# Kernel optimization log

Measured on AMD Instinct MI355X. Metric: run time of the kernel, lower is better.

The kernel has to match this reference:

```python
import jax, jax.numpy as jnp
import numpy as np

NHEADS = 4


def mha(q, k, v, w_in, b_in, w_out, b_out):
    # torch.nn.MultiheadAttention (batch_first): packed in_proj then out_proj
    B, Nq, E = q.shape
    d = E // NHEADS
    wq, wk, wv = jnp.split(w_in, 3, axis=0)
    bq, bk, bv = jnp.split(b_in, 3)
    qh = (q @ wq.T + bq).reshape(B, Nq, NHEADS, d)
    kh = (k @ wk.T + bk).reshape(B, k.shape[1], NHEADS, d)
    vh = (v @ wv.T + bv).reshape(B, v.shape[1], NHEADS, d)
    scores = jnp.einsum('bqhd,bkhd->bhqk', qh, kh) * (1.0 / np.float32(np.sqrt(d)))
    attn = jax.nn.softmax(scores, axis=-1)
    out = jnp.einsum('bhqk,bkhd->bqhd', attn, vh).reshape(B, Nq, E)
    return out @ w_out.T + b_out


def kabsch(A, B):
    # n_dim_rigid_transform_Kabsch_3D_torch; note: reflect() in the source sets
    # SS = identity on BOTH branches, so it is a no-op and R = U @ Vt exactly.
    cA = A.mean(1, keepdims=True)   # [B,1,3]
    cB = B.mean(1, keepdims=True)
    Am = A - cA
    Bm = B - cB
    H = jnp.einsum('bni,bnj->bij', Bm, Am)  # Bm^T @ Am, [B,3,3]
    U, S, Vt = jnp.linalg.svd(H, full_matrices=False)
    R = U @ Vt
    t = cA - cB @ R
    return R, t


def setup_inputs() -> dict:
    key = jax.random.key(0)
    ks = jax.random.split(key, 32)
    B, N, F, E = 64, 512, 16, 12

    def p(k, shape, s=0.1):
        return jax.random.normal(k, shape, jnp.float32) * s

    inp = {}
    inp['x_orig'] = jax.random.normal(ks[0], (B, N, F), jnp.float32)
    inp['y_orig'] = jax.random.normal(ks[1], (B, N, F), jnp.float32)
    inp['lin_in_w'] = p(ks[2], (E, F - 3))
    inp['lin_in_b'] = p(ks[3], (E,))
    inp['lin_coords_w'] = p(ks[4], (E, 3))
    inp['lin_coords_b'] = p(ks[5], (E,))
    for i, name in enumerate(['attn', 'attn_feat', 'cross_cf', 'cross']):
        b = 6 + 4 * i
        inp[name + '_w_in'] = p(ks[b], (3 * E, E))
        inp[name + '_b_in'] = p(ks[b + 1], (3 * E,))
        inp[name + '_w_out'] = p(ks[b + 2], (E, E))
        inp[name + '_b_out'] = p(ks[b + 3], (E,))
    inp['lin_out_w'] = p(ks[22], (3, E))
    inp['lin_out_b'] = p(ks[23], (3,))
    return inp


def reference(x_orig, y_orig,
              lin_in_w, lin_in_b, lin_coords_w, lin_coords_b,
              attn_w_in, attn_b_in, attn_w_out, attn_b_out,
              attn_feat_w_in, attn_feat_b_in, attn_feat_w_out, attn_feat_b_out,
              cross_cf_w_in, cross_cf_b_in, cross_cf_w_out, cross_cf_b_out,
              cross_w_in, cross_b_in, cross_w_out, cross_b_out,
              lin_out_w, lin_out_b):
    x_coords = x_orig[:, :, :3]
    x_feat = x_orig[:, :, 3:]
    y_coords = y_orig[:, :, :3]
    y_feat = y_orig[:, :, 3:]

    x_coords = x_coords - x_coords.mean(1, keepdims=True)
    y_translate = y_coords.mean(1, keepdims=True)
    y_coords = y_coords - y_translate

    xi = x_coords @ lin_coords_w.T + lin_coords_b
    yi = y_coords @ lin_coords_w.T + lin_coords_b
    xi_feat = x_feat @ lin_in_w.T + lin_in_b
    yi_feat = y_feat @ lin_in_w.T + lin_in_b

    xi_feat = mha(xi_feat, xi_feat, xi_feat, attn_feat_w_in, attn_feat_b_in, attn_feat_w_out, attn_feat_b_out)
    yi_feat = mha(yi_feat, yi_feat, yi_feat, attn_feat_w_in, attn_feat_b_in, attn_feat_w_out, attn_feat_b_out)
    xi = mha(xi, xi, xi, attn_w_in, attn_b_in, attn_w_out, attn_b_out)
    yi = mha(yi, yi, yi, attn_w_in, attn_b_in, attn_w_out, attn_b_out)

    cross_x = mha(xi, xi_feat, xi_feat, cross_cf_w_in, cross_cf_b_in, cross_cf_w_out, cross_cf_b_out)
    cross_y = mha(yi, yi_feat, yi_feat, cross_cf_w_in, cross_cf_b_in, cross_cf_w_out, cross_cf_b_out)
    cross = mha(cross_x, cross_y, cross_y, cross_w_in, cross_b_in, cross_w_out, cross_b_out)

    coords = cross @ lin_out_w.T + lin_out_b  # [B,N,3]
    R, t = kabsch(coords + x_coords, x_coords)
    return x_coords @ R + t + y_translate
```

## Files before the change

kernel.cpp:

```cpp
#include <hip/hip_runtime.h>
#include <hip/hip_fp16.h>
#include <math.h>

#define NB 64
#define NN 512
#define NE 12
#define NH 4
#define NF 13

typedef __attribute__((ext_vector_type(4))) _Float16 f16x4;
typedef __attribute__((ext_vector_type(4))) float    f32x4;

__device__ inline float wave_reduce_add(float v) {
#pragma unroll
    for (int off = 1; off < 64; off <<= 1) v += __shfl_xor(v, off);
    return v;
}

__device__ inline unsigned h2u(__half2 h) { union { __half2 h; unsigned u; } c; c.h = h; return c.u; }

union HU { f16x4 h; uint2 u; };

__global__ __launch_bounds__(512) void prep_kernel(
    const float* __restrict__ x_orig, const float* __restrict__ y_orig,
    const float* __restrict__ lin_in_w, const float* __restrict__ lin_in_b,
    const float* __restrict__ lin_coords_w, const float* __restrict__ lin_coords_b,
    float* __restrict__ x_c, float* __restrict__ y_tr,
    float* __restrict__ xi, float* __restrict__ yi,
    float* __restrict__ xi_feat, float* __restrict__ yi_feat)
{
    const int b = blockIdx.x;
    const int n = threadIdx.x;
    const size_t row = (size_t)b * NN + n;
    const float* xr = x_orig + row * 16;
    const float* yr = y_orig + row * 16;
    float xv[16], yv[16];
#pragma unroll
    for (int i = 0; i < 16; ++i) { xv[i] = xr[i]; yv[i] = yr[i]; }

    __shared__ float part[8][6];
    const int wid = n >> 6, lane = n & 63;
    float r0 = wave_reduce_add(xv[0]);
    float r1 = wave_reduce_add(xv[1]);
    float r2 = wave_reduce_add(xv[2]);
    float r3 = wave_reduce_add(yv[0]);
    float r4 = wave_reduce_add(yv[1]);
    float r5 = wave_reduce_add(yv[2]);
    if (lane == 0) {
        part[wid][0] = r0; part[wid][1] = r1; part[wid][2] = r2;
        part[wid][3] = r3; part[wid][4] = r4; part[wid][5] = r5;
    }
    __syncthreads();
    float xm[3], ym[3];
#pragma unroll
    for (int c = 0; c < 3; ++c) {
        float sx = 0.f, sy = 0.f;
#pragma unroll
        for (int w = 0; w < 8; ++w) { sx += part[w][c]; sy += part[w][3 + c]; }
        xm[c] = sx * (1.0f / NN); ym[c] = sy * (1.0f / NN);
    }

    float xc[3], yc[3];
#pragma unroll
    for (int c = 0; c < 3; ++c) { xc[c] = xv[c] - xm[c]; yc[c] = yv[c] - ym[c]; }

#pragma unroll
    for (int c = 0; c < 3; ++c) x_c[row * 3 + c] = xc[c];
    if (n < 3) y_tr[b * 3 + n] = ym[n];

#pragma unroll
    for (int e = 0; e < NE; ++e) {
        float sx = lin_coords_b[e], sy = lin_coords_b[e];
#pragma unroll
        for (int c = 0; c < 3; ++c) {
            sx += xc[c] * lin_coords_w[e * 3 + c];
            sy += yc[c] * lin_coords_w[e * 3 + c];
        }
        xi[row * NE + e] = sx;
        yi[row * NE + e] = sy;
    }
#pragma unroll
    for (int e = 0; e < NE; ++e) {
        float sx = lin_in_b[e], sy = lin_in_b[e];
#pragma unroll
        for (int f = 0; f < NF; ++f) {
            sx += xv[3 + f] * lin_in_w[e * NF + f];
            sy += yv[3 + f] * lin_in_w[e * NF + f];
        }
        xi_feat[row * NE + e] = sx;
        yi_feat[row * NE + e] = sy;
    }
}

struct MhaBatchArgs {
    const float* q[4];
    const float* kv[4];
    const float* wi[4];
    const float* bi[4];
    const float* wo[4];
    const float* bo[4];
    float*       out[4];
};

__global__ __launch_bounds__(512) void attn_mfma_kernel(MhaBatchArgs args)
{
    const int op    = blockIdx.x >> 8;
    const int bid   = blockIdx.x & 255;
    const int b     = bid >> 2;
    const int qbase = (bid & 3) << 7;
    const int tid   = threadIdx.x;
    const int lane  = tid & 63;
    const int w     = tid >> 6;
    const int h     = w >> 1;
    const int q64   = w & 1;

    const float* __restrict__ qin   = args.q[op];
    const float* __restrict__ kvin  = args.kv[op];
    const float* __restrict__ w_in  = args.wi[op];
    const float* __restrict__ b_in  = args.bi[op];
    const float* __restrict__ w_out = args.wo[op];
    const float* __restrict__ b_out = args.bo[op];
    float* __restrict__ out = args.out[op];

    __shared__ __align__(16) __half K_lds[NH][NN][4];
    __shared__ __align__(16) __half V_lds[NH][4][528];
    __shared__ __align__(16) __half Q_lds[128][NH][4];
    __shared__ __align__(16) float  att[128][NE];
    __shared__ float  w_lds[36][NE];
    __shared__ float  b_lds[36];
    __shared__ __align__(16) float4 wo4[NE][3];
    __shared__ float  bo_lds[NE];

    if (tid < 432) w_lds[tid / NE][tid % NE] = w_in[tid];
    if (tid < 36)  b_lds[tid] = b_in[tid];
    if (tid < 144) ((float*)wo4)[tid] = w_out[tid];
    if (tid < NE)  bo_lds[tid] = b_out[tid];
    __syncthreads();

    {
        const int n = tid;
        const float4* kvrow = (const float4*)(kvin + ((size_t)b * NN + n) * NE);
        float4 r0 = kvrow[0], r1 = kvrow[1], r2 = kvrow[2];
        float x[NE] = { r0.x, r0.y, r0.z, r0.w, r1.x, r1.y, r1.z, r1.w,
                        r2.x, r2.y, r2.z, r2.w };
#pragma unroll
        for (int hh = 0; hh < NH; ++hh) {
            float sk[3], sv[3];
#pragma unroll
            for (int c = 0; c < 3; ++c) {
                const int rk = NE + hh * 3 + c;
                const int rv = 2 * NE + hh * 3 + c;
                float a = b_lds[rk], v = b_lds[rv];
#pragma unroll
                for (int e = 0; e < NE; ++e) {
                    a += x[e] * w_lds[rk][e];
                    v += x[e] * w_lds[rv][e];
                }
                sk[c] = a; sv[c] = v;
            }
            uint2 kk;
            kk.x = h2u(__floats2half2_rn(sk[0], sk[1]));
            kk.y = h2u(__floats2half2_rn(sk[2], 0.0f));
            *(uint2*)&K_lds[hh][n][0] = kk;
            V_lds[hh][0][n] = __float2half(sv[0]);
            V_lds[hh][1][n] = __float2half(sv[1]);
            V_lds[hh][2][n] = __float2half(sv[2]);
            V_lds[hh][3][n] = __float2half(1.0f);
        }
    }
    {
        const float scale = 0.83294037f;
        const int q = tid >> 2, hh = tid & 3;
        const float4* qrow = (const float4*)(qin + ((size_t)b * NN + qbase + q) * NE);
        float4 r0 = qrow[0], r1 = qrow[1], r2 = qrow[2];
        float x[NE] = { r0.x, r0.y, r0.z, r0.w, r1.x, r1.y, r1.z, r1.w,
                        r2.x, r2.y, r2.z, r2.w };
        float qc[3];
#pragma unroll
        for (int c = 0; c < 3; ++c) {
            const int rq = hh * 3 + c;
            float s = b_lds[rq];
#pragma unroll
            for (int e = 0; e < NE; ++e) s += x[e] * w_lds[rq][e];
            qc[c] = s * scale;
        }
        uint2 qq;
        qq.x = h2u(__floats2half2_rn(qc[0], qc[1]));
        qq.y = h2u(__floats2half2_rn(qc[2], 0.0f));
        *(uint2*)&Q_lds[q][hh][0] = qq;
    }
    __syncthreads();

    const int ql = lane & 15;
    const int g  = lane >> 4;
    f16x4 qf[4];
#pragma unroll
    for (int j = 0; j < 4; ++j) {
        HU c;
        c.u = *(const uint2*)&Q_lds[q64 * 64 + j * 16 + ql][h][0];
        if (lane >= 16) { c.u.x = 0u; c.u.y = 0u; }
        qf[j] = c.h;
    }
    f32x4 acc[4];
#pragma unroll
    for (int j = 0; j < 4; ++j) acc[j] = (f32x4){0.f, 0.f, 0.f, 0.f};

    const f32x4 zero4 = {0.f, 0.f, 0.f, 0.f};

    for (int ks = 0; ks < 32; ++ks) {
        HU kc; kc.u = *(const uint2*)&K_lds[h][ks * 16 + ql][0];
        HU vc; vc.u = *(const uint2*)&V_lds[h][lane & 3][ks * 16 + 4 * g];
#pragma unroll
        for (int j = 0; j < 4; ++j) {
            f32x4 s = __builtin_amdgcn_mfma_f32_16x16x16f16(kc.h, qf[j], zero4, 0, 0, 0);
            float p0 = __builtin_amdgcn_exp2f(s[0]);
            float p1 = __builtin_amdgcn_exp2f(s[1]);
            float p2 = __builtin_amdgcn_exp2f(s[2]);
            float p3 = __builtin_amdgcn_exp2f(s[3]);
            HU pc;
            pc.u.x = h2u(__floats2half2_rn(p0, p1));
            pc.u.y = h2u(__floats2half2_rn(p2, p3));
            acc[j] = __builtin_amdgcn_mfma_f32_16x16x16f16(vc.h, pc.h, acc[j], 0, 0, 0);
        }
    }

    if (lane < 16) {
#pragma unroll
        for (int j = 0; j < 4; ++j) {
            const int qloc = q64 * 64 + j * 16 + lane;
            const float inv = 1.0f / acc[j][3];
            att[qloc][h * 3 + 0] = acc[j][0] * inv;
            att[qloc][h * 3 + 1] = acc[j][1] * inv;
            att[qloc][h * 3 + 2] = acc[j][2] * inv;
        }
    }
    __syncthreads();

    for (int idx = tid; idx < 128 * NE; idx += 512) {
        const int qq = idx / NE, o = idx % NE;
        const float4* a4 = (const float4*)&att[qq][0];
        float4 a0 = a4[0], a1 = a4[1], a2 = a4[2];
        float4 w0 = wo4[o][0], w1 = wo4[o][1], w2 = wo4[o][2];
        float s = bo_lds[o]
                + a0.x * w0.x + a0.y * w0.y + a0.z * w0.z + a0.w * w0.w
                + a1.x * w1.x + a1.y * w1.y + a1.z * w1.z + a1.w * w1.w
                + a2.x * w2.x + a2.y * w2.y + a2.z * w2.z + a2.w * w2.w;
        out[((size_t)b * NN + qbase + qq) * NE + o] = s;
    }
}

__global__ __launch_bounds__(512) void kabsch_accum_kernel(
    const float* __restrict__ cross, const float* __restrict__ lin_out_w,
    const float* __restrict__ lin_out_b, const float* __restrict__ x_c,
    float* __restrict__ stats)
{
    const int b = blockIdx.x;
    const int n = threadIdx.x;
    const size_t row = (size_t)b * NN + n;
    const float* xr = cross + row * NE;
    float xin[NE];
#pragma unroll
    for (int e = 0; e < NE; ++e) xin[e] = xr[e];
    float cd[3];
#pragma unroll
    for (int o = 0; o < 3; ++o) {
        float s = lin_out_b[o];
#pragma unroll
        for (int e = 0; e < NE; ++e) s += xin[e] * lin_out_w[o * NE + e];
        cd[o] = s;
    }
    float Bx[3], A[3];
#pragma unroll
    for (int c = 0; c < 3; ++c) { Bx[c] = x_c[row * 3 + c]; A[c] = cd[c] + Bx[c]; }

    float vals[15];
#pragma unroll
    for (int i = 0; i < 3; ++i)
#pragma unroll
        for (int j = 0; j < 3; ++j) vals[i * 3 + j] = Bx[i] * A[j];
#pragma unroll
    for (int i = 0; i < 3; ++i) { vals[9 + i] = Bx[i]; vals[12 + i] = A[i]; }

    __shared__ float part[8][15];
    const int wid = n >> 6, lane = n & 63;
#pragma unroll
    for (int t = 0; t < 15; ++t) {
        float r = wave_reduce_add(vals[t]);
        if (lane == 0) part[wid][t] = r;
    }
    __syncthreads();
    if (n < 15) {
        float s = 0.f;
#pragma unroll
        for (int w = 0; w < 8; ++w) s += part[w][n];
        stats[b * 15 + n] = s;
    }
}

__global__ __launch_bounds__(64) void kabsch_r_kernel(
    const float* __restrict__ stats, float* __restrict__ Rb, float* __restrict__ tb)
{
    const int b = threadIdx.x;
    if (b >= NB) return;
    const float* s = stats + b * 15;
    float cB[3], cA[3];
#pragma unroll
    for (int j = 0; j < 3; ++j) { cB[j] = s[9 + j] * (1.0f / NN); cA[j] = s[12 + j] * (1.0f / NN); }
    float X[3][3];
#pragma unroll
    for (int i = 0; i < 3; ++i)
#pragma unroll
        for (int j = 0; j < 3; ++j) X[i][j] = s[i * 3 + j] - s[9 + i] * cA[j];

    for (int it = 0; it < 14; ++it) {
        float c00 =  X[1][1] * X[2][2] - X[1][2] * X[2][1];
        float c01 = -(X[1][0] * X[2][2] - X[1][2] * X[2][0]);
        float c02 =  X[1][0] * X[2][1] - X[1][1] * X[2][0];
        float c10 = -(X[0][1] * X[2][2] - X[0][2] * X[2][1]);
        float c11 =  X[0][0] * X[2][2] - X[0][2] * X[2][0];
        float c12 = -(X[0][0] * X[2][1] - X[0][1] * X[2][0]);
        float c20 =  X[0][1] * X[1][2] - X[0][2] * X[1][1];
        float c21 = -(X[0][0] * X[1][2] - X[0][2] * X[1][0]);
        float c22 =  X[0][0] * X[1][1] - X[0][1] * X[1][0];
        float det = X[0][0] * c00 + X[0][1] * c01 + X[0][2] * c02;
        float ad = fabsf(det);
        float g  = (ad > 1e-30f) ? 1.0f / cbrtf(ad) : 1.0f;
        float hg  = 0.5f * g;
        float hgi = 0.5f / (g * det);
        float Xn[3][3];
        Xn[0][0] = hg * X[0][0] + hgi * c00;
        Xn[0][1] = hg * X[0][1] + hgi * c01;
        Xn[0][2] = hg * X[0][2] + hgi * c02;
        Xn[1][0] = hg * X[1][0] + hgi * c10;
        Xn[1][1] = hg * X[1][1] + hgi * c11;
        Xn[1][2] = hg * X[1][2] + hgi * c12;
        Xn[2][0] = hg * X[2][0] + hgi * c20;
        Xn[2][1] = hg * X[2][1] + hgi * c21;
        Xn[2][2] = hg * X[2][2] + hgi * c22;
#pragma unroll
        for (int i = 0; i < 3; ++i)
#pragma unroll
            for (int j = 0; j < 3; ++j) X[i][j] = Xn[i][j];
    }
#pragma unroll
    for (int i = 0; i < 3; ++i)
#pragma unroll
        for (int j = 0; j < 3; ++j) Rb[b * 9 + i * 3 + j] = X[i][j];
#pragma unroll
    for (int j = 0; j < 3; ++j)
        tb[b * 3 + j] = cA[j] - (cB[0] * X[0][j] + cB[1] * X[1][j] + cB[2] * X[2][j]);
}

__global__ __launch_bounds__(256) void final_kernel(
    const float* __restrict__ x_c, const float* __restrict__ Rb,
    const float* __restrict__ tb, const float* __restrict__ y_tr,
    float* __restrict__ out)
{
    const int row = blockIdx.x * 256 + threadIdx.x;
    if (row >= NB * NN) return;
    const int b = row >> 9;
    const float* R = Rb + b * 9;
    const float* t = tb + b * 3;
    const float* yt = y_tr + b * 3;
    float x0 = x_c[(size_t)row * 3 + 0];
    float x1 = x_c[(size_t)row * 3 + 1];
    float x2 = x_c[(size_t)row * 3 + 2];
#pragma unroll
    for (int j = 0; j < 3; ++j) {
        out[(size_t)row * 3 + j] = x0 * R[j] + x1 * R[3 + j] + x2 * R[6 + j] + t[j] + yt[j];
    }
}

extern "C" void kernel_launch(void* const* d_in, const int* in_sizes, int n_in,
                              void* d_out, int out_size, void* d_ws, size_t ws_size,
                              hipStream_t stream)
{
    const float* x_orig       = (const float*)d_in[0];
    const float* y_orig       = (const float*)d_in[1];
    const float* lin_in_w     = (const float*)d_in[2];
    const float* lin_in_b     = (const float*)d_in[3];
    const float* lin_coords_w = (const float*)d_in[4];
    const float* lin_coords_b = (const float*)d_in[5];
    const float* attn_w_in    = (const float*)d_in[6];
    const float* attn_b_in    = (const float*)d_in[7];
    const float* attn_w_out   = (const float*)d_in[8];
    const float* attn_b_out   = (const float*)d_in[9];
    const float* af_w_in      = (const float*)d_in[10];
    const float* af_b_in      = (const float*)d_in[11];
    const float* af_w_out     = (const float*)d_in[12];
    const float* af_b_out     = (const float*)d_in[13];
    const float* ccf_w_in     = (const float*)d_in[14];
    const float* ccf_b_in     = (const float*)d_in[15];
    const float* ccf_w_out    = (const float*)d_in[16];
    const float* ccf_b_out    = (const float*)d_in[17];
    const float* cr_w_in      = (const float*)d_in[18];
    const float* cr_b_in      = (const float*)d_in[19];
    const float* cr_w_out     = (const float*)d_in[20];
    const float* cr_b_out     = (const float*)d_in[21];
    const float* lin_out_w    = (const float*)d_in[22];
    const float* lin_out_b    = (const float*)d_in[23];

    float* ws = (float*)d_ws;
    const size_t BN3 = (size_t)NB * NN * 3;
    const size_t BNE = (size_t)NB * NN * NE;

    float* x_c   = ws;
    float* y_tr  = x_c + BN3;
    float* A     = y_tr + 192;
    float* B     = A + BNE;
    float* C     = B + BNE;
    float* D     = C + BNE;
    float* E0    = D + BNE;
    float* E1    = E0 + BNE;
    float* E2    = E1 + BNE;
    float* E3    = E2 + BNE;

    const size_t batch_floats = BN3 + 192 + 8 * BNE + NB * (15 + 9 + 3);
    const bool batched = ws_size >= batch_floats * sizeof(float);

    float* stats = (batched ? E3 + BNE : E0 + BNE);
    float* Rb    = stats + NB * 15;
    float* tb    = Rb + NB * 9;

    prep_kernel<<<NB, 512, 0, stream>>>(x_orig, y_orig, lin_in_w, lin_in_b,
                                        lin_coords_w, lin_coords_b,
                                        x_c, y_tr, A, B, C, D);

    auto set_op = [](MhaBatchArgs& a, int i, const float* q, const float* kv,
                     const float* wi, const float* bi,
                     const float* wo, const float* bo, float* o) {
        a.q[i] = q; a.kv[i] = kv; a.wi[i] = wi; a.bi[i] = bi;
        a.wo[i] = wo; a.bo[i] = bo; a.out[i] = o;
    };

    if (batched) {
        MhaBatchArgs a1{};
        set_op(a1, 0, C, C, af_w_in, af_b_in, af_w_out, af_b_out, E0);
        set_op(a1, 1, D, D, af_w_in, af_b_in, af_w_out, af_b_out, E1);
        set_op(a1, 2, A, A, attn_w_in, attn_b_in, attn_w_out, attn_b_out, E2);
        set_op(a1, 3, B, B, attn_w_in, attn_b_in, attn_w_out, attn_b_out, E3);
        attn_mfma_kernel<<<4 * 256, 512, 0, stream>>>(a1);
        MhaBatchArgs a2{};
        set_op(a2, 0, E2, E0, ccf_w_in, ccf_b_in, ccf_w_out, ccf_b_out, A);
        set_op(a2, 1, E3, E1, ccf_w_in, ccf_b_in, ccf_w_out, ccf_b_out, B);
        attn_mfma_kernel<<<2 * 256, 512, 0, stream>>>(a2);
        MhaBatchArgs a3{};
        set_op(a3, 0, A, B, cr_w_in, cr_b_in, cr_w_out, cr_b_out, C);
        attn_mfma_kernel<<<256, 512, 0, stream>>>(a3);
        kabsch_accum_kernel<<<NB, 512, 0, stream>>>(C, lin_out_w, lin_out_b, x_c, stats);
    } else {
        auto mha1 = [&](const float* q, const float* kv,
                        const float* wi, const float* bi,
                        const float* wo, const float* bo, float* o) {
            MhaBatchArgs a{};
            set_op(a, 0, q, kv, wi, bi, wo, bo, o);
            attn_mfma_kernel<<<256, 512, 0, stream>>>(a);
        };
        mha1(C, C, af_w_in, af_b_in, af_w_out, af_b_out, E0);
        mha1(D, D, af_w_in, af_b_in, af_w_out, af_b_out, C);
        mha1(A, A, attn_w_in, attn_b_in, attn_w_out, attn_b_out, D);
        mha1(B, B, attn_w_in, attn_b_in, attn_w_out, attn_b_out, A);
        mha1(D, E0, ccf_w_in, ccf_b_in, ccf_w_out, ccf_b_out, B);
        mha1(A, C, ccf_w_in, ccf_b_in, ccf_w_out, ccf_b_out, E0);
        mha1(B, E0, cr_w_in, cr_b_in, cr_w_out, cr_b_out, C);
        kabsch_accum_kernel<<<NB, 512, 0, stream>>>(C, lin_out_w, lin_out_b, x_c, stats);
    }

    kabsch_r_kernel<<<1, 64, 0, stream>>>(stats, Rb, tb);
    final_kernel<<<(NB * NN) / 256, 256, 0, stream>>>(x_c, Rb, tb, y_tr, (float*)d_out);
}
```

Before: 99.24 us.

## Precompute K/V projections once per batch in a separate kernel before attention

Adds a proj_kv_kernel that computes the fp16 K and V projections once per batch element and writes them to workspace. Before this, each of the four query-block workgroups of a batch recomputed the projections itself. The attention kernel now loads the staged K/V instead. Shared memory is also reduced by reusing the Q buffer as fp16 attention-output storage. The cost is extra kernel launches, extra global traffic for the staged buffers, and the attention output now held in fp16 before out_proj, which loses some precision.

```diff
diff --git a/kernel.cpp b/kernel.cpp
--- a/kernel.cpp
+++ b/kernel.cpp
@@ -18,6 +18,7 @@
 }
 
 __device__ inline unsigned h2u(__half2 h) { union { __half2 h; unsigned u; } c; c.h = h; return c.u; }
+__device__ inline __half2 u2h2(unsigned u) { union { __half2 h; unsigned u; } c; c.u = u; return c.h; }
 
 union HU { f16x4 h; uint2 u; };
 
@@ -92,6 +93,61 @@
     }
 }
 
+struct ProjArgs {
+    const float* kv[4];
+    const float* wi[4];
+    const float* bi[4];
+    uint2*       ks[4];
+    uint2*       vs[4];
+};
+
+__global__ __launch_bounds__(512) void proj_kv_kernel(ProjArgs pa)
+{
+    const int op = blockIdx.x >> 6;
+    const int b  = blockIdx.x & 63;
+    const int n  = threadIdx.x;
+    const float* __restrict__ kvin = pa.kv[op];
+    const float* __restrict__ w_in = pa.wi[op];
+    const float* __restrict__ b_in = pa.bi[op];
+
+    __shared__ float w_lds[36][NE];
+    __shared__ float b_lds[36];
+    if (n < 432) w_lds[n / NE][n % NE] = w_in[n];
+    if (n < 36)  b_lds[n] = b_in[n];
+    __syncthreads();
+
+    const float4* kvrow = (const float4*)(kvin + ((size_t)b * NN + n) * NE);
+    float4 r0 = kvrow[0], r1 = kvrow[1], r2 = kvrow[2];
+    float x[NE] = { r0.x, r0.y, r0.z, r0.w, r1.x, r1.y, r1.z, r1.w,
+                    r2.x, r2.y, r2.z, r2.w };
+    uint2* ko = pa.ks[op];
+    uint2* vo = pa.vs[op];
+    const int idx = b * NN + n;
+#pragma unroll
+    for (int hh = 0; hh < NH; ++hh) {
+        float sk[3], sv[3];
+#pragma unroll
+        for (int c = 0; c < 3; ++c) {
+            const int rk = NE + hh * 3 + c;
+            const int rv = 2 * NE + hh * 3 + c;
+            float a = b_lds[rk], v = b_lds[rv];
+#pragma unroll
+            for (int e = 0; e < NE; ++e) {
+                a += x[e] * w_lds[rk][e];
+                v += x[e] * w_lds[rv][e];
+            }
+            sk[c] = a; sv[c] = v;
+        }
+        uint2 kk, vv;
+        kk.x = h2u(__floats2half2_rn(sk[0], sk[1]));
+        kk.y = h2u(__floats2half2_rn(sk[2], 0.0f));
+        vv.x = h2u(__floats2half2_rn(sv[0], sv[1]));
+        vv.y = h2u(__floats2half2_rn(sv[2], 1.0f));
+        ko[hh * (NB * NN) + idx] = kk;
+        vo[hh * (NB * NN) + idx] = vv;
+    }
+}
+
 struct MhaBatchArgs {
     const float* q[4];
     const float* kv[4];
@@ -100,8 +156,11 @@
     const float* wo[4];
     const float* bo[4];
     float*       out[4];
+    const uint2* ks[4];
+    const uint2* vs[4];
 };
 
+template<bool STAGED>
 __global__ __launch_bounds__(512) void attn_mfma_kernel(MhaBatchArgs args)
 {
     const int op    = blockIdx.x >> 8;
@@ -115,7 +174,6 @@
     const int q64   = w & 1;
 
     const float* __restrict__ qin   = args.q[op];
-    const float* __restrict__ kvin  = args.kv[op];
     const float* __restrict__ w_in  = args.wi[op];
     const float* __restrict__ b_in  = args.bi[op];
     const float* __restrict__ w_out = args.wo[op];
@@ -124,8 +182,7 @@
 
     __shared__ __align__(16) __half K_lds[NH][NN][4];
     __shared__ __align__(16) __half V_lds[NH][4][528];
-    __shared__ __align__(16) __half Q_lds[128][NH][4];
-    __shared__ __align__(16) float  att[128][NE];
+    __shared__ __align__(16) uint2  qbuf[128][NH];
     __shared__ float  w_lds[36][NE];
     __shared__ float  b_lds[36];
     __shared__ __align__(16) float4 wo4[NE][3];
@@ -137,7 +194,24 @@
     if (tid < NE)  bo_lds[tid] = b_out[tid];
     __syncthreads();
 
-    {
+    if (STAGED) {
+        const uint2* __restrict__ Ks = args.ks[op];
+        const uint2* __restrict__ Vs = args.vs[op];
+        const int n = tid;
+        const int idx = b * NN + n;
+#pragma unroll
+        for (int hh = 0; hh < NH; ++hh) {
+            uint2 kk = Ks[hh * (NB * NN) + idx];
+            *(uint2*)&K_lds[hh][n][0] = kk;
+            uint2 vv = Vs[hh * (NB * NN) + idx];
+            __half2 vxy = u2h2(vv.x), vz1 = u2h2(vv.y);
+            V_lds[hh][0][n] = __low2half(vxy);
+            V_lds[hh][1][n] = __high2half(vxy);
+            V_lds[hh][2][n] = __low2half(vz1);
+            V_lds[hh][3][n] = __high2half(vz1);
+        }
+    } else {
+        const float* __restrict__ kvin = args.kv[op];
         const int n = tid;
         const float4* kvrow = (const float4*)(kvin + ((size_t)b * NN + n) * NE);
         float4 r0 = kvrow[0], r1 = kvrow[1], r2 = kvrow[2];
@@ -187,7 +261,7 @@
         uint2 qq;
         qq.x = h2u(__floats2half2_rn(qc[0], qc[1]));
         qq.y = h2u(__floats2half2_rn(qc[2], 0.0f));
-        *(uint2*)&Q_lds[q][hh][0] = qq;
+        qbuf[q][hh] = qq;
     }
     __syncthreads();
 
@@ -197,7 +271,7 @@
 #pragma unroll
     for (int j = 0; j < 4; ++j) {
         HU c;
-        c.u = *(const uint2*)&Q_lds[q64 * 64 + j * 16 + ql][h][0];
+        c.u = qbuf[q64 * 64 + j * 16 + ql][h];
         if (lane >= 16) { c.u.x = 0u; c.u.y = 0u; }
         qf[j] = c.h;
     }
@@ -224,27 +298,30 @@
         }
     }
 
+    __syncthreads();
+    __half* att = (__half*)qbuf;
     if (lane < 16) {
 #pragma unroll
         for (int j = 0; j < 4; ++j) {
             const int qloc = q64 * 64 + j * 16 + lane;
             const float inv = 1.0f / acc[j][3];
-            att[qloc][h * 3 + 0] = acc[j][0] * inv;
-            att[qloc][h * 3 + 1] = acc[j][1] * inv;
-            att[qloc][h * 3 + 2] = acc[j][2] * inv;
+            att[qloc * NE + h * 3 + 0] = __float2half(acc[j][0] * inv);
+            att[qloc * NE + h * 3 + 1] = __float2half(acc[j][1] * inv);
+            att[qloc * NE + h * 3 + 2] = __float2half(acc[j][2] * inv);
         }
     }
     __syncthreads();
 
     for (int idx = tid; idx < 128 * NE; idx += 512) {
         const int qq = idx / NE, o = idx % NE;
-        const float4* a4 = (const float4*)&att[qq][0];
-        float4 a0 = a4[0], a1 = a4[1], a2 = a4[2];
-        float4 w0 = wo4[o][0], w1 = wo4[o][1], w2 = wo4[o][2];
-        float s = bo_lds[o]
-                + a0.x * w0.x + a0.y * w0.y + a0.z * w0.z + a0.w * w0.w
-                + a1.x * w1.x + a1.y * w1.y + a1.z * w1.z + a1.w * w1.w
-                + a2.x * w2.x + a2.y * w2.y + a2.z * w2.z + a2.w * w2.w;
+        const __half2* arow = (const __half2*)&att[qq * NE];
+        const float* wrow = (const float*)&wo4[o][0];
+        float s = bo_lds[o];
+#pragma unroll
+        for (int m = 0; m < 6; ++m) {
+            float2 fv = __half22float2(arow[m]);
+            s += fv.x * wrow[2 * m] + fv.y * wrow[2 * m + 1];
+        }
         out[((size_t)b * NN + qbase + qq) * NE + o] = s;
     }
 }
@@ -403,6 +480,7 @@
     float* ws = (float*)d_ws;
     const size_t BN3 = (size_t)NB * NN * 3;
     const size_t BNE = (size_t)NB * NN * NE;
+    const size_t BNN = (size_t)NB * NN;
 
     float* x_c   = ws;
     float* y_tr  = x_c + BN3;
@@ -415,22 +493,35 @@
     float* E2    = E1 + BNE;
     float* E3    = E2 + BNE;
 
-    const size_t batch_floats = BN3 + 192 + 8 * BNE + NB * (15 + 9 + 3);
-    const bool batched = ws_size >= batch_floats * sizeof(float);
+    const size_t base_floats = BN3 + 192 + 8 * BNE + NB * (15 + 9 + 3);
+    const size_t staged_bytes = base_floats * sizeof(float) + 8 * (size_t)NH * BNN * 8;
+    const bool batched = ws_size >= base_floats * sizeof(float);
+    const bool staged  = ws_size >= staged_bytes;
 
     float* stats = (batched ? E3 + BNE : E0 + BNE);
     float* Rb    = stats + NB * 15;
     float* tb    = Rb + NB * 9;
 
+    uint2* Ks_all = (uint2*)(ws + base_floats);
+    uint2* Vs_all = Ks_all + 4 * (size_t)NH * BNN;
+
     prep_kernel<<<NB, 512, 0, stream>>>(x_orig, y_orig, lin_in_w, lin_in_b,
                                         lin_coords_w, lin_coords_b,
                                         x_c, y_tr, A, B, C, D);
 
-    auto set_op = [](MhaBatchArgs& a, int i, const float* q, const float* kv,
-                     const float* wi, const float* bi,
-                     const float* wo, const float* bo, float* o) {
+    auto set_op = [&](MhaBatchArgs& a, int i, const float* q, const float* kv,
+                      const float* wi, const float* bi,
+                      const float* wo, const float* bo, float* o) {
         a.q[i] = q; a.kv[i] = kv; a.wi[i] = wi; a.bi[i] = bi;
         a.wo[i] = wo; a.bo[i] = bo; a.out[i] = o;
+        a.ks[i] = Ks_all + (size_t)i * NH * BNN;
+        a.vs[i] = Vs_all + (size_t)i * NH * BNN;
+    };
+    auto set_proj = [&](ProjArgs& p, int i, const float* kv,
+                        const float* wi, const float* bi) {
+        p.kv[i] = kv; p.wi[i] = wi; p.bi[i] = bi;
+        p.ks[i] = Ks_all + (size_t)i * NH * BNN;
+        p.vs[i] = Vs_all + (size_t)i * NH * BNN;
     };
 
     if (batched) {
@@ -439,14 +530,34 @@
         set_op(a1, 1, D, D, af_w_in, af_b_in, af_w_out, af_b_out, E1);
         set_op(a1, 2, A, A, attn_w_in, attn_b_in, attn_w_out, attn_b_out, E2);
         set_op(a1, 3, B, B, attn_w_in, attn_b_in, attn_w_out, attn_b_out, E3);
-        attn_mfma_kernel<<<4 * 256, 512, 0, stream>>>(a1);
         MhaBatchArgs a2{};
         set_op(a2, 0, E2, E0, ccf_w_in, ccf_b_in, ccf_w_out, ccf_b_out, A);
         set_op(a2, 1, E3, E1, ccf_w_in, ccf_b_in, ccf_w_out, ccf_b_out, B);
-        attn_mfma_kernel<<<2 * 256, 512, 0, stream>>>(a2);
         MhaBatchArgs a3{};
         set_op(a3, 0, A, B, cr_w_in, cr_b_in, cr_w_out, cr_b_out, C);
-        attn_mfma_kernel<<<256, 512, 0, stream>>>(a3);
+
+        if (staged) {
+            ProjArgs p1{};
+            set_proj(p1, 0, C, af_w_in, af_b_in);
+            set_proj(p1, 1, D, af_w_in, af_b_in);
+            set_proj(p1, 2, A, attn_w_in, attn_b_in);
+            set_proj(p1, 3, B, attn_w_in, attn_b_in);
+            proj_kv_kernel<<<4 * NB, 512, 0, stream>>>(p1);
+            attn_mfma_kernel<true><<<4 * 256, 512, 0, stream>>>(a1);
+            ProjArgs p2{};
+            set_proj(p2, 0, E0, ccf_w_in, ccf_b_in);
+            set_proj(p2, 1, E1, ccf_w_in, ccf_b_in);
+            proj_kv_kernel<<<2 * NB, 512, 0, stream>>>(p2);
+            attn_mfma_kernel<true><<<2 * 256, 512, 0, stream>>>(a2);
+            ProjArgs p3{};
+            set_proj(p3, 0, B, cr_w_in, cr_b_in);
+            proj_kv_kernel<<<NB, 512, 0, stream>>>(p3);
+            attn_mfma_kernel<true><<<256, 512, 0, stream>>>(a3);
+        } else {
+            attn_mfma_kernel<false><<<4 * 256, 512, 0, stream>>>(a1);
+            attn_mfma_kernel<false><<<2 * 256, 512, 0, stream>>>(a2);
+            attn_mfma_kernel<false><<<256, 512, 0, stream>>>(a3);
+        }
         kabsch_accum_kernel<<<NB, 512, 0, stream>>>(C, lin_out_w, lin_out_b, x_c, stats);
     } else {
         auto mha1 = [&](const float* q, const float* kv,
@@ -454,7 +565,7 @@
                         const float* wo, const float* bo, float* o) {
             MhaBatchArgs a{};
             set_op(a, 0, q, kv, wi, bi, wo, bo, o);
-            attn_mfma_kernel<<<256, 512, 0, stream>>>(a);
+            attn_mfma_kernel<false><<<256, 512, 0, stream>>>(a);
         };
         mha1(C, C, af_w_in, af_b_in, af_w_out, af_b_out, E0);
         mha1(D, D, af_w_in, af_b_in, af_w_out, af_b_out, C);
```

Result: slower. 112.5 us (+13.3%).

## Fuse Kabsch accumulation, rotation solve and final transform into one kernel

Applied to the files above, without the earlier changes.

Merges the per-batch stats reduction, the 3x3 polar-decomposition iteration and the final rotation/translation apply into a single kernel per batch. Thread 0 of each block solves R and t into shared memory, and every thread then applies the transform to its own row. This removes two kernel launches and the global round trips for stats, R and t. It also unrolls the attention key loop by two and retypes the Q shared buffer as uint2. The cost is a serial 14-iteration solve on one thread per block while the other threads wait.

```diff
diff --git a/kernel.cpp b/kernel.cpp
--- a/kernel.cpp
+++ b/kernel.cpp
@@ -124,7 +124,7 @@
 
     __shared__ __align__(16) __half K_lds[NH][NN][4];
     __shared__ __align__(16) __half V_lds[NH][4][528];
-    __shared__ __align__(16) __half Q_lds[128][NH][4];
+    __shared__ __align__(16) uint2  qbuf[128][NH];
     __shared__ __align__(16) float  att[128][NE];
     __shared__ float  w_lds[36][NE];
     __shared__ float  b_lds[36];
@@ -187,7 +187,7 @@
         uint2 qq;
         qq.x = h2u(__floats2half2_rn(qc[0], qc[1]));
         qq.y = h2u(__floats2half2_rn(qc[2], 0.0f));
-        *(uint2*)&Q_lds[q][hh][0] = qq;
+        qbuf[q][hh] = qq;
     }
     __syncthreads();
 
@@ -197,7 +197,7 @@
 #pragma unroll
     for (int j = 0; j < 4; ++j) {
         HU c;
-        c.u = *(const uint2*)&Q_lds[q64 * 64 + j * 16 + ql][h][0];
+        c.u = qbuf[q64 * 64 + j * 16 + ql][h];
         if (lane >= 16) { c.u.x = 0u; c.u.y = 0u; }
         qf[j] = c.h;
     }
@@ -207,6 +207,7 @@
 
     const f32x4 zero4 = {0.f, 0.f, 0.f, 0.f};
 
+#pragma unroll 2
     for (int ks = 0; ks < 32; ++ks) {
         HU kc; kc.u = *(const uint2*)&K_lds[h][ks * 16 + ql][0];
         HU vc; vc.u = *(const uint2*)&V_lds[h][lane & 3][ks * 16 + 4 * g];
@@ -249,10 +250,10 @@
     }
 }
 
-__global__ __launch_bounds__(512) void kabsch_accum_kernel(
+__global__ __launch_bounds__(512) void kabsch_fused_kernel(
     const float* __restrict__ cross, const float* __restrict__ lin_out_w,
     const float* __restrict__ lin_out_b, const float* __restrict__ x_c,
-    float* __restrict__ stats)
+    const float* __restrict__ y_tr, float* __restrict__ out)
 {
     const int b = blockIdx.x;
     const int n = threadIdx.x;
@@ -282,6 +283,7 @@
     for (int i = 0; i < 3; ++i) { vals[9 + i] = Bx[i]; vals[12 + i] = A[i]; }
 
     __shared__ float part[8][15];
+    __shared__ float Rt[12];
     const int wid = n >> 6, lane = n & 63;
 #pragma unroll
     for (int t = 0; t < 15; ++t) {
@@ -289,85 +291,70 @@
         if (lane == 0) part[wid][t] = r;
     }
     __syncthreads();
-    if (n < 15) {
-        float s = 0.f;
-#pragma unroll
-        for (int w = 0; w < 8; ++w) s += part[w][n];
-        stats[b * 15 + n] = s;
-    }
-}
-
-__global__ __launch_bounds__(64) void kabsch_r_kernel(
-    const float* __restrict__ stats, float* __restrict__ Rb, float* __restrict__ tb)
-{
-    const int b = threadIdx.x;
-    if (b >= NB) return;
-    const float* s = stats + b * 15;
-    float cB[3], cA[3];
-#pragma unroll
-    for (int j = 0; j < 3; ++j) { cB[j] = s[9 + j] * (1.0f / NN); cA[j] = s[12 + j] * (1.0f / NN); }
-    float X[3][3];
-#pragma unroll
-    for (int i = 0; i < 3; ++i)
-#pragma unroll
-        for (int j = 0; j < 3; ++j) X[i][j] = s[i * 3 + j] - s[9 + i] * cA[j];
-
-    for (int it = 0; it < 14; ++it) {
-        float c00 =  X[1][1] * X[2][2] - X[1][2] * X[2][1];
-        float c01 = -(X[1][0] * X[2][2] - X[1][2] * X[2][0]);
-        float c02 =  X[1][0] * X[2][1] - X[1][1] * X[2][0];
-        float c10 = -(X[0][1] * X[2][2] - X[0][2] * X[2][1]);
-        float c11 =  X[0][0] * X[2][2] - X[0][2] * X[2][0];
-        float c12 = -(X[0][0] * X[2][1] - X[0][1] * X[2][0]);
-        float c20 =  X[0][1] * X[1][2] - X[0][2] * X[1][1];
-        float c21 = -(X[0][0] * X[1][2] - X[0][2] * X[1][0]);
-        float c22 =  X[0][0] * X[1][1] - X[0][1] * X[1][0];
-        float det = X[0][0] * c00 + X[0][1] * c01 + X[0][2] * c02;
-        float ad = fabsf(det);
-        float g  = (ad > 1e-30f) ? 1.0f / cbrtf(ad) : 1.0f;
-        float hg  = 0.5f * g;
-        float hgi = 0.5f / (g * det);
-        float Xn[3][3];
-        Xn[0][0] = hg * X[0][0] + hgi * c00;
-        Xn[0][1] = hg * X[0][1] + hgi * c01;
-        Xn[0][2] = hg * X[0][2] + hgi * c02;
-        Xn[1][0] = hg * X[1][0] + hgi * c10;
-        Xn[1][1] = hg * X[1][1] + hgi * c11;
-        Xn[1][2] = hg * X[1][2] + hgi * c12;
-        Xn[2][0] = hg * X[2][0] + hgi * c20;
-        Xn[2][1] = hg * X[2][1] + hgi * c21;
-        Xn[2][2] = hg * X[2][2] + hgi * c22;
+
+    if (n == 0) {
+        float s[15];
+#pragma unroll
+        for (int t = 0; t < 15; ++t) {
+            float acc = 0.f;
+#pragma unroll
+            for (int ww = 0; ww < 8; ++ww) acc += part[ww][t];
+            s[t] = acc;
+        }
+        float cB[3], cA[3];
+#pragma unroll
+        for (int j = 0; j < 3; ++j) { cB[j] = s[9 + j] * (1.0f / NN); cA[j] = s[12 + j] * (1.0f / NN); }
+        float X[3][3];
 #pragma unroll
         for (int i = 0; i < 3; ++i)
 #pragma unroll
-            for (int j = 0; j < 3; ++j) X[i][j] = Xn[i][j];
-    }
-#pragma unroll
-    for (int i = 0; i < 3; ++i)
-#pragma unroll
-        for (int j = 0; j < 3; ++j) Rb[b * 9 + i * 3 + j] = X[i][j];
-#pragma unroll
-    for (int j = 0; j < 3; ++j)
-        tb[b * 3 + j] = cA[j] - (cB[0] * X[0][j] + cB[1] * X[1][j] + cB[2] * X[2][j]);
-}
-
-__global__ __launch_bounds__(256) void final_kernel(
-    const float* __restrict__ x_c, const float* __restrict__ Rb,
-    const float* __restrict__ tb, const float* __restrict__ y_tr,
-    float* __restrict__ out)
-{
-    const int row = blockIdx.x * 256 + threadIdx.x;
-    if (row >= NB * NN) return;
-    const int b = row >> 9;
-    const float* R = Rb + b * 9;
-    const float* t = tb + b * 3;
-    const float* yt = y_tr + b * 3;
-    float x0 = x_c[(size_t)row * 3 + 0];
-    float x1 = x_c[(size_t)row * 3 + 1];
-    float x2 = x_c[(size_t)row * 3 + 2];
+            for (int j = 0; j < 3; ++j) X[i][j] = s[i * 3 + j] - s[9 + i] * cA[j];
+
+        for (int it = 0; it < 14; ++it) {
+            float c00 =  X[1][1] * X[2][2] - X[1][2] * X[2][1];
+            float c01 = -(X[1][0] * X[2][2] - X[1][2] * X[2][0]);
+            float c02 =  X[1][0] * X[2][1] - X[1][1] * X[2][0];
+            float c10 = -(X[0][1] * X[2][2] - X[0][2] * X[2][1]);
+            float c11 =  X[0][0] * X[2][2] - X[0][2] * X[2][0];
+            float c12 = -(X[0][0] * X[2][1] - X[0][1] * X[2][0]);
+            float c20 =  X[0][1] * X[1][2] - X[0][2] * X[1][1];
+            float c21 = -(X[0][0] * X[1][2] - X[0][2] * X[1][0]);
+            float c22 =  X[0][0] * X[1][1] - X[0][1] * X[1][0];
+            float det = X[0][0] * c00 + X[0][1] * c01 + X[0][2] * c02;
+            float ad = fabsf(det);
+            float g  = (ad > 1e-30f) ? 1.0f / cbrtf(ad) : 1.0f;
+            float hg  = 0.5f * g;
+            float hgi = 0.5f / (g * det);
+            float Xn[3][3];
+            Xn[0][0] = hg * X[0][0] + hgi * c00;
+            Xn[0][1] = hg * X[0][1] + hgi * c01;
+            Xn[0][2] = hg * X[0][2] + hgi * c02;
+            Xn[1][0] = hg * X[1][0] + hgi * c10;
+            Xn[1][1] = hg * X[1][1] + hgi * c11;
+            Xn[1][2] = hg * X[1][2] + hgi * c12;
+            Xn[2][0] = hg * X[2][0] + hgi * c20;
+            Xn[2][1] = hg * X[2][1] + hgi * c21;
+            Xn[2][2] = hg * X[2][2] + hgi * c22;
+#pragma unroll
+            for (int i = 0; i < 3; ++i)
+#pragma unroll
+                for (int j = 0; j < 3; ++j) X[i][j] = Xn[i][j];
+        }
+#pragma unroll
+        for (int i = 0; i < 3; ++i)
+#pragma unroll
+            for (int j = 0; j < 3; ++j) Rt[i * 3 + j] = X[i][j];
+#pragma unroll
+        for (int j = 0; j < 3; ++j)
+            Rt[9 + j] = cA[j] - (cB[0] * X[0][j] + cB[1] * X[1][j] + cB[2] * X[2][j])
+                      + y_tr[b * 3 + j];
+    }
+    __syncthreads();
+
+    const float x0 = Bx[0], x1 = Bx[1], x2 = Bx[2];
 #pragma unroll
     for (int j = 0; j < 3; ++j) {
-        out[(size_t)row * 3 + j] = x0 * R[j] + x1 * R[3 + j] + x2 * R[6 + j] + t[j] + yt[j];
+        out[row * 3 + j] = x0 * Rt[j] + x1 * Rt[3 + j] + x2 * Rt[6 + j] + Rt[9 + j];
     }
 }
 
@@ -418,10 +405,6 @@
     const size_t batch_floats = BN3 + 192 + 8 * BNE + NB * (15 + 9 + 3);
     const bool batched = ws_size >= batch_floats * sizeof(float);
 
-    float* stats = (batched ? E3 + BNE : E0 + BNE);
-    float* Rb    = stats + NB * 15;
-    float* tb    = Rb + NB * 9;
-
     prep_kernel<<<NB, 512, 0, stream>>>(x_orig, y_orig, lin_in_w, lin_in_b,
                                         lin_coords_w, lin_coords_b,
                                         x_c, y_tr, A, B, C, D);
@@ -447,7 +430,8 @@
         MhaBatchArgs a3{};
         set_op(a3, 0, A, B, cr_w_in, cr_b_in, cr_w_out, cr_b_out, C);
         attn_mfma_kernel<<<256, 512, 0, stream>>>(a3);
-        kabsch_accum_kernel<<<NB, 512, 0, stream>>>(C, lin_out_w, lin_out_b, x_c, stats);
+        kabsch_fused_kernel<<<NB, 512, 0, stream>>>(C, lin_out_w, lin_out_b,
+                                                    x_c, y_tr, (float*)d_out);
     } else {
         auto mha1 = [&](const float* q, const float* kv,
                         const float* wi, const float* bi,
@@ -463,9 +447,7 @@
         mha1(D, E0, ccf_w_in, ccf_b_in, ccf_w_out, ccf_b_out, B);
         mha1(A, C, ccf_w_in, ccf_b_in, ccf_w_out, ccf_b_out, E0);
         mha1(B, E0, cr_w_in, cr_b_in, cr_w_out, cr_b_out, C);
-        kabsch_accum_kernel<<<NB, 512, 0, stream>>>(C, lin_out_w, lin_out_b, x_c, stats);
-    }
-
-    kabsch_r_kernel<<<1, 64, 0, stream>>>(stats, Rb, tb);
-    final_kernel<<<(NB * NN) / 256, 256, 0, stream>>>(x_c, Rb, tb, y_tr, (float*)d_out);
+        kabsch_fused_kernel<<<NB, 512, 0, stream>>>(C, lin_out_w, lin_out_b,
+                                                    x_c, y_tr, (float*)d_out);
+    }
 }
```

Result: faster. 96.52 us (-2.7%).
